# Optimization experiments

Hardware: AMD Instinct MI355X
Metric: run time of the kernel (lower is better)

Reference implementation:

```python
import jax, jax.numpy as jnp
import numpy as np

B, S, D_IN, D_OUT = 4, 2048, 4096, 4096


def setup_inputs() -> dict:
    key = jax.random.key(0)
    k1, k2, k3, k4 = jax.random.split(key, 4)
    x = jax.random.normal(k1, (B, S, D_IN), dtype=jnp.float32)
    # int8-valued weights stored as int32 (values in [-127, 127])
    weight_int8 = jax.random.randint(k2, (D_OUT, D_IN), -127, 128, dtype=jnp.int32)
    # per-output-channel scale, strictly positive (abs-max / 127 style)
    scale = jax.random.uniform(k3, (D_OUT, 1), dtype=jnp.float32, minval=1e-4, maxval=2e-2)
    bias = jax.random.normal(k4, (D_OUT,), dtype=jnp.float32)
    return {"x": x, "weight_int8": weight_int8, "scale": scale, "bias": bias}


def reference(x, weight_int8, scale, bias):
    # Dequantize: per-output-row scale applied to int8 weights -> fp32 [O, I]
    w = weight_int8.astype(jnp.float32) * scale
    # F.linear: y = x @ w^T + b
    out = jnp.einsum('bsi,oi->bso', x, w) + bias
    return out
```

## Files before the change

### kernel.cpp

```cpp
#include <hip/hip_runtime.h>
#include <hip/hip_bf16.h>
#include <cstdint>
#include <cstddef>

typedef int  i32x4 __attribute__((ext_vector_type(4)));

#define BM 128
#define BN 128
#define BK 64

__device__ __forceinline__ void load16_to_lds(const void* g, void* l) {
  __builtin_amdgcn_global_load_lds(
      (const __attribute__((address_space(1))) void*)g,
      (__attribute__((address_space(3))) void*)l,
      16, 0, 0);
}

__global__ __launch_bounds__(256) void quant_x(const float* __restrict__ x,
                                               char* __restrict__ xq,
                                               float* __restrict__ sx,
                                               int K ) {
  const int row = blockIdx.x;
  const int t   = threadIdx.x;
  const float* xr = x + (size_t)row * K;
  float4 v[4];
  float amax = 0.f;
#pragma unroll
  for (int j = 0; j < 4; ++j) {
    v[j] = ((const float4*)xr)[t + j * 256];
    amax = fmaxf(amax, fmaxf(fmaxf(fabsf(v[j].x), fabsf(v[j].y)),
                             fmaxf(fabsf(v[j].z), fabsf(v[j].w))));
  }
#pragma unroll
  for (int off = 32; off; off >>= 1)
    amax = fmaxf(amax, __shfl_xor(amax, off));
  __shared__ float red[4];
  if ((t & 63) == 0) red[t >> 6] = amax;
  __syncthreads();
  amax = fmaxf(fmaxf(red[0], red[1]), fmaxf(red[2], red[3]));
  amax = fmaxf(amax, 1e-20f);

  const float s = 127.0f / amax;
  int* outw = (int*)(xq + (size_t)row * K);
#pragma unroll
  for (int j = 0; j < 4; ++j) {
    int q0 = __float2int_rn(v[j].x * s);
    int q1 = __float2int_rn(v[j].y * s);
    int q2 = __float2int_rn(v[j].z * s);
    int q3 = __float2int_rn(v[j].w * s);
    int pk = (q0 & 0xff) | ((q1 & 0xff) << 8) | ((q2 & 0xff) << 16) | ((q3 & 0xff) << 24);
    outw[t + j * 256] = pk;
  }
  if (t == 0) sx[row] = amax * (1.0f / 127.0f);
}

__global__ __launch_bounds__(256) void quant_w(const int* __restrict__ w,
                                               char* __restrict__ wq) {
  const size_t base = (size_t)blockIdx.x * 4096;
  const int t = threadIdx.x;
  int* outw = (int*)(wq + base);
#pragma unroll
  for (int j = 0; j < 4; ++j) {
    const int c = t + j * 256;
    int4 a = ((const int4*)(w + base))[c];
    outw[c] = (a.x & 0xff) | ((a.y & 0xff) << 8) | ((a.z & 0xff) << 16) | ((a.w & 0xff) << 24);
  }
}

__global__ __launch_bounds__(256) void gemm_i8_bt(const char* __restrict__ A,
                                                  const char* __restrict__ Bw,
                                                  const float* __restrict__ sx,
                                                  const float* __restrict__ sw,
                                                  const float* __restrict__ bias,
                                                  float* __restrict__ out,
                                                  int M, int N, int K) {
  __shared__ char As[BM * BK];
  __shared__ char Bs[BN * BK];

  const int tid  = threadIdx.x;
  const int wave = tid >> 6;
  const int lane = tid & 63;
  const int wm   = wave >> 1;
  const int wn   = wave & 1;
  const int bm   = blockIdx.y;
  const int bn   = blockIdx.x;

  i32x4 acc[4][4] = {};

  const int rowT = tid >> 2;
  const int colg = (tid & 3) * 16;
  const char* Ag1 = A  + (size_t)(bm * BM + rowT) * K + colg;
  const char* Ag2 = Ag1 + (size_t)64 * K;
  const char* Bg1 = Bw + (size_t)(bn * BN + rowT) * K + colg;
  const char* Bg2 = Bg1 + (size_t)64 * K;

  char* AsW1 = As + wave * 1024;
  char* AsW2 = As + 4096 + wave * 1024;
  char* BsW1 = Bs + wave * 1024;
  char* BsW2 = Bs + 4096 + wave * 1024;

  const int fr   = lane & 15;
  const int kq16 = (lane >> 4) * 16;

  for (int k0 = 0; k0 < K; k0 += BK) {
    load16_to_lds(Ag1 + k0, AsW1);
    load16_to_lds(Ag2 + k0, AsW2);
    load16_to_lds(Bg1 + k0, BsW1);
    load16_to_lds(Bg2 + k0, BsW2);
    __syncthreads();

    i32x4 af[4], bf[4];
#pragma unroll
    for (int i = 0; i < 4; ++i) {
      af[i] = *(const i32x4*)&As[(wm * 64 + i * 16 + fr) * BK + kq16];
      bf[i] = *(const i32x4*)&Bs[(wn * 64 + i * 16 + fr) * BK + kq16];
    }
#pragma unroll
    for (int m = 0; m < 4; ++m)
#pragma unroll
      for (int n = 0; n < 4; ++n)
        acc[m][n] = __builtin_amdgcn_mfma_i32_16x16x64_i8(af[m], bf[n], acc[m][n], 0, 0, 0);

    __syncthreads();
  }

  const int colc = lane & 15;
  const int rq   = (lane >> 4) * 4;
#pragma unroll
  for (int n = 0; n < 4; ++n) {
    const int col = bn * BN + wn * 64 + n * 16 + colc;
    const float sc = sw[col];
    const float bi = bias[col];
#pragma unroll
    for (int m = 0; m < 4; ++m) {
      const int row0 = bm * BM + wm * 64 + m * 16 + rq;
#pragma unroll
      for (int r = 0; r < 4; ++r) {
        const int row = row0 + r;
        out[(size_t)row * N + col] = (float)acc[m][n][r] * (sx[row] * sc) + bi;
      }
    }
  }
}

extern "C" void kernel_launch(void* const* d_in, const int* in_sizes, int n_in,
                              void* d_out, int out_size, void* d_ws, size_t ws_size,
                              hipStream_t stream) {
  const float* x     = (const float*)d_in[0];
  const int*   w     = (const int*)d_in[1];
  const float* scale = (const float*)d_in[2];
  const float* bias  = (const float*)d_in[3];
  float*       out   = (float*)d_out;

  const int N = in_sizes[3];
  const int K = in_sizes[1] / N;
  const int M = in_sizes[0] / K;

  char*  xq = (char*)d_ws;
  char*  wq = xq + (size_t)M * K;
  float* sx = (float*)(wq + (size_t)N * K);

  quant_x<<<dim3(M), dim3(256), 0, stream>>>(x, xq, sx, K);
  quant_w<<<dim3((unsigned)(((size_t)N * K) / 4096)), dim3(256), 0, stream>>>(w, wq);

  gemm_i8_bt<<<dim3(N / BN, M / BM), dim3(256), 0, stream>>>(xq, wq, sx, scale, bias, out, M, N, K);
}
```

Before: 467.9 us.

## Double-buffer LDS tiles and XOR-swizzle int8 GEMM shared-memory layout

The int8 GEMM now keeps two LDS buffers for A and B. It prefetches the next K-tile with global_load_lds while running the MFMAs on the current tile, which removes one barrier per iteration and hides global latency behind compute. The global source column is XOR-permuted by row and the LDS reads apply the matching swizzle, to cut bank conflicts on the 16-byte fragment reads. In exchange, LDS use per block doubles, which may lower occupancy.

```diff
diff --git a/kernel.cpp b/kernel.cpp
--- a/kernel.cpp
+++ b/kernel.cpp
@@ -74,8 +74,8 @@
                                                   const float* __restrict__ bias,
                                                   float* __restrict__ out,
                                                   int M, int N, int K) {
-  __shared__ char As[BM * BK];
-  __shared__ char Bs[BN * BK];
+  __shared__ char As[2][BM * BK];
+  __shared__ char Bs[2][BN * BK];
 
   const int tid  = threadIdx.x;
   const int wave = tid >> 6;
@@ -88,32 +88,45 @@
   i32x4 acc[4][4] = {};
 
   const int rowT = tid >> 2;
-  const int colg = (tid & 3) * 16;
-  const char* Ag1 = A  + (size_t)(bm * BM + rowT) * K + colg;
+  const int jg   = ((tid & 3) ^ ((tid >> 3) & 3)) * 16;
+  const char* Ag1 = A  + (size_t)(bm * BM + rowT) * K + jg;
   const char* Ag2 = Ag1 + (size_t)64 * K;
-  const char* Bg1 = Bw + (size_t)(bn * BN + rowT) * K + colg;
+  const char* Bg1 = Bw + (size_t)(bn * BN + rowT) * K + jg;
   const char* Bg2 = Bg1 + (size_t)64 * K;
 
-  char* AsW1 = As + wave * 1024;
-  char* AsW2 = As + 4096 + wave * 1024;
-  char* BsW1 = Bs + wave * 1024;
-  char* BsW2 = Bs + 4096 + wave * 1024;
+  const int ldsOff1 = wave * 1024;
+  const int ldsOff2 = 4096 + wave * 1024;
 
-  const int fr   = lane & 15;
-  const int kq16 = (lane >> 4) * 16;
+  const int fr  = lane & 15;
+  const int swz = ((lane >> 4) ^ ((fr >> 1) & 3)) * 16;
+  int offA[4], offB[4];
+#pragma unroll
+  for (int i = 0; i < 4; ++i) {
+    offA[i] = (wm * 64 + i * 16 + fr) * 64 + swz;
+    offB[i] = (wn * 64 + i * 16 + fr) * 64 + swz;
+  }
 
+  load16_to_lds(Ag1, &As[0][ldsOff1]);
+  load16_to_lds(Ag2, &As[0][ldsOff2]);
+  load16_to_lds(Bg1, &Bs[0][ldsOff1]);
+  load16_to_lds(Bg2, &Bs[0][ldsOff2]);
+
+  int kb = 0;
   for (int k0 = 0; k0 < K; k0 += BK) {
-    load16_to_lds(Ag1 + k0, AsW1);
-    load16_to_lds(Ag2 + k0, AsW2);
-    load16_to_lds(Bg1 + k0, BsW1);
-    load16_to_lds(Bg2 + k0, BsW2);
     __syncthreads();
+
+    if (k0 + BK < K) {
+      load16_to_lds(Ag1 + k0 + BK, &As[kb ^ 1][ldsOff1]);
+      load16_to_lds(Ag2 + k0 + BK, &As[kb ^ 1][ldsOff2]);
+      load16_to_lds(Bg1 + k0 + BK, &Bs[kb ^ 1][ldsOff1]);
+      load16_to_lds(Bg2 + k0 + BK, &Bs[kb ^ 1][ldsOff2]);
+    }
 
     i32x4 af[4], bf[4];
 #pragma unroll
     for (int i = 0; i < 4; ++i) {
-      af[i] = *(const i32x4*)&As[(wm * 64 + i * 16 + fr) * BK + kq16];
-      bf[i] = *(const i32x4*)&Bs[(wn * 64 + i * 16 + fr) * BK + kq16];
+      af[i] = *(const i32x4*)&As[kb][offA[i]];
+      bf[i] = *(const i32x4*)&Bs[kb][offB[i]];
     }
 #pragma unroll
     for (int m = 0; m < 4; ++m)
@@ -121,7 +134,7 @@
       for (int n = 0; n < 4; ++n)
         acc[m][n] = __builtin_amdgcn_mfma_i32_16x16x64_i8(af[m], bf[n], acc[m][n], 0, 0, 0);
 
-    __syncthreads();
+    kb ^= 1;
   }
 
   const int colc = lane & 15;
```

New measurement: 450.5 us. -3.7%, faster.
